# Kernel tuning notes

Hardware: AMD Instinct MI355X
Metric: run time of the kernel (lower is better)

Reference implementation:

```python
import jax, jax.numpy as jnp
import numpy as np


def setup_inputs() -> dict:
    key = jax.random.key(0)
    k1, k2, k3, k4 = jax.random.split(key, 4)
    N, E, D = 50000, 800000, 256
    x = jax.random.normal(k1, (N, D), dtype=jnp.float32)
    edge_index = jax.random.randint(k2, (2, E), 0, N, dtype=jnp.int64)
    W = jax.random.normal(k3, (D, D), dtype=jnp.float32) * (1.0 / np.sqrt(D))
    b_conv = jnp.zeros((D,), dtype=jnp.float32)
    w_lin = jax.random.normal(k4, (1, D), dtype=jnp.float32) * (1.0 / np.sqrt(D))
    b_lin = jnp.zeros((1,), dtype=jnp.float32)
    return {"x": x, "edge_index": edge_index, "W": W, "b_conv": b_conv,
            "w_lin": w_lin, "b_lin": b_lin}


def reference(x, edge_index, W, b_conv, w_lin, b_lin):
    N = x.shape[0]
    # GCNConv with add_self_loops=True, symmetric normalization
    loop = jnp.arange(N, dtype=edge_index.dtype)
    row = jnp.concatenate([edge_index[0], loop])  # source
    col = jnp.concatenate([edge_index[1], loop])  # target
    ones = jnp.ones(row.shape[0], dtype=x.dtype)
    deg = jax.ops.segment_sum(ones, col, num_segments=N)
    deg_inv_sqrt = jnp.where(deg > 0, jax.lax.rsqrt(deg), 0.0)
    norm = deg_inv_sqrt[row] * deg_inv_sqrt[col]  # [E+N]
    h = x @ W                                      # [N, D]
    msg = h[row] * norm[:, None]                   # [E+N, D]
    agg = jax.ops.segment_sum(msg, col, num_segments=N) + b_conv  # [N, D]
    x1 = jax.nn.sigmoid(agg)
    # dropout is identity in eval mode
    x3 = jnp.mean(x1, axis=0)                      # [D]
    x4 = jax.nn.sigmoid(x3 @ w_lin.T + b_lin)      # [1]
    return x4
```

## Files before the change

### kernel.cpp

```cpp
#include <hip/hip_runtime.h>
#include <hip/hip_bf16.h>
#include <stdint.h>

typedef short bf16x8 __attribute__((ext_vector_type(8)));
typedef unsigned short u16x8 __attribute__((ext_vector_type(8)));
typedef float f32x4 __attribute__((ext_vector_type(4)));

static __device__ __forceinline__ unsigned short f32_to_bf16_bits(float f) {
    union { float f; uint32_t u; } v; v.f = f;
    uint32_t lsb = (v.u >> 16) & 1u;
    uint32_t r = v.u + 0x7fffu + lsb;
    return (unsigned short)(r >> 16);
}
static __device__ __forceinline__ float bf16_bits_to_f32(unsigned short u) {
    union { uint32_t u; float f; } v; v.u = ((uint32_t)u) << 16;
    return v.f;
}

__global__ void count_kernel(const int* __restrict__ col, int* __restrict__ cnt, int E) {
    int e = blockIdx.x * blockDim.x + threadIdx.x;
    if (e < E) atomicAdd(&cnt[col[e]], 1);
}

__global__ void scanA_kernel(const int* __restrict__ cnt, int* __restrict__ off,
                             int* __restrict__ bsums, int N) {
    int tid = threadIdx.x;
    int b = blockIdx.x;
    int i0 = b * 1024 + tid * 4;
    int v0 = (i0 + 0 < N) ? cnt[i0 + 0] : 0;
    int v1 = (i0 + 1 < N) ? cnt[i0 + 1] : 0;
    int v2 = (i0 + 2 < N) ? cnt[i0 + 2] : 0;
    int v3 = (i0 + 3 < N) ? cnt[i0 + 3] : 0;
    int s = v0 + v1 + v2 + v3;
    int lane = tid & 63, wid = tid >> 6;
    int inc = s;
    for (int d = 1; d < 64; d <<= 1) {
        int o = __shfl_up(inc, d, 64);
        if (lane >= d) inc += o;
    }
    __shared__ int wt[4];
    if (lane == 63) wt[wid] = inc;
    __syncthreads();
    int wbase = 0;
    for (int k = 0; k < wid; k++) wbase += wt[k];
    int excl = wbase + inc - s;
    if (i0 + 0 < N) off[i0 + 0] = excl;
    if (i0 + 1 < N) off[i0 + 1] = excl + v0;
    if (i0 + 2 < N) off[i0 + 2] = excl + v0 + v1;
    if (i0 + 3 < N) off[i0 + 3] = excl + v0 + v1 + v2;
    if (tid == 255) bsums[b] = wbase + inc;
}

__global__ void scanB_kernel(const int* __restrict__ bsums, int* __restrict__ bbase, int nb) {
    int t = threadIdx.x;
    int s = (t < nb) ? bsums[t] : 0;
    int inc = s;
    for (int d = 1; d < 64; d <<= 1) {
        int o = __shfl_up(inc, d, 64);
        if (t >= d) inc += o;
    }
    if (t < nb) bbase[t] = inc - s;
}

__global__ void scanC_kernel(int* __restrict__ off, int* __restrict__ cursor,
                             float* __restrict__ dis, const int* __restrict__ cnt,
                             const int* __restrict__ bbase, int N, int E) {
    int i = blockIdx.x * blockDim.x + threadIdx.x;
    if (i < N) {
        int o = off[i] + bbase[i >> 10];
        off[i] = o;
        cursor[i] = o;
        dis[i] = rsqrtf((float)(cnt[i] + 1));
    }
    if (i == 0) off[N] = E;
}

__global__ void scatter_kernel(const int* __restrict__ ei, int* __restrict__ cursor,
                               int* __restrict__ srow, int E) {
    int e = blockIdx.x * blockDim.x + threadIdx.x;
    if (e < E) {
        int r = ei[e];
        int c = ei[E + e];
        int p = atomicAdd(&cursor[c], 1);
        srow[p] = r;
    }
}

__global__ __launch_bounds__(256) void xconv_kernel(const float* __restrict__ x,
                                                    unsigned short* __restrict__ xb, int total8) {
    int stride = gridDim.x * blockDim.x;
    for (int i = blockIdx.x * blockDim.x + threadIdx.x; i < total8; i += stride) {
        const float* p = x + (size_t)i * 8;
        float4 a = *(const float4*)p;
        float4 b = *(const float4*)(p + 4);
        u16x8 o;
        o[0] = f32_to_bf16_bits(a.x); o[1] = f32_to_bf16_bits(a.y);
        o[2] = f32_to_bf16_bits(a.z); o[3] = f32_to_bf16_bits(a.w);
        o[4] = f32_to_bf16_bits(b.x); o[5] = f32_to_bf16_bits(b.y);
        o[6] = f32_to_bf16_bits(b.z); o[7] = f32_to_bf16_bits(b.w);
        *(u16x8*)(xb + (size_t)i * 8) = o;
    }
}

__global__ void wprep_kernel(const float* __restrict__ W, unsigned short* __restrict__ Wb) {
    int e = blockIdx.x * blockDim.x + threadIdx.x;
    int k = e >> 8, n = e & 255;
    Wb[(((k >> 3) * 256 + n) << 3) + (k & 7)] = f32_to_bf16_bits(W[e]);
}

__global__ __launch_bounds__(256) void gemm_kernel(const unsigned short* __restrict__ xb,
                                                   const unsigned short* __restrict__ Wb,
                                                   unsigned short* __restrict__ h, int N) {
    int tid = threadIdx.x;
    int lane = tid & 63;
    int w = tid >> 6;
    int l15 = lane & 15, l4 = lane >> 4;
    int m0 = blockIdx.x * 64;
    int colbase = w * 64;

    f32x4 acc[4][4];
    for (int mi = 0; mi < 4; mi++)
        for (int ni = 0; ni < 4; ni++)
            acc[mi][ni] = (f32x4){0.f, 0.f, 0.f, 0.f};

    for (int kk = 0; kk < 8; kk++) {
        bf16x8 a[4], bb[4];
        int k0 = kk * 32 + l4 * 8;
        for (int mi = 0; mi < 4; mi++) {
            int row = m0 + mi * 16 + l15;
            if (row >= N) row = N - 1;
            a[mi] = *(const bf16x8*)(xb + (size_t)row * 256 + k0);
        }
        int kc = kk * 4 + l4;
        for (int ni = 0; ni < 4; ni++) {
            int n = colbase + ni * 16 + l15;
            bb[ni] = *(const bf16x8*)(Wb + (((kc << 8) + n) << 3));
        }
        for (int mi = 0; mi < 4; mi++)
            for (int ni = 0; ni < 4; ni++)
                acc[mi][ni] = __builtin_amdgcn_mfma_f32_16x16x32_bf16(a[mi], bb[ni], acc[mi][ni], 0, 0, 0);
    }

    __shared__ unsigned short tile[4 * 64 * 72];
    unsigned short* tw = tile + w * 64 * 72;
    for (int mi = 0; mi < 4; mi++)
        for (int ni = 0; ni < 4; ni++)
            for (int v = 0; v < 4; v++)
                tw[(mi * 16 + l4 * 4 + v) * 72 + ni * 16 + l15] = f32_to_bf16_bits(acc[mi][ni][v]);
    __builtin_amdgcn_s_waitcnt(0);
    for (int t = 0; t < 8; t++) {
        int row_r = t * 8 + (lane >> 3);
        int col_r = (lane & 7) * 8;
        int gr = m0 + row_r;
        if (gr < N) {
            u16x8 vv = *(const u16x8*)(tw + row_r * 72 + col_r);
            *(u16x8*)(h + (size_t)gr * 256 + colbase + col_r) = vv;
        }
    }
}

__global__ __launch_bounds__(256) void agg_kernel(const unsigned short* __restrict__ h,
                                                  const int* __restrict__ off,
                                                  const int* __restrict__ srow,
                                                  const float* __restrict__ dis,
                                                  const float* __restrict__ bconv,
                                                  float* __restrict__ partials, int N) {
    int lane = threadIdx.x & 63, wid = threadIdx.x >> 6;
    int hi = lane >> 5;
    int l5 = lane & 31;
    int c8 = l5 * 8;
    float bc[8];
    {
        float4 b0 = *(const float4*)(bconv + c8);
        float4 b1 = *(const float4*)(bconv + c8 + 4);
        bc[0]=b0.x; bc[1]=b0.y; bc[2]=b0.z; bc[3]=b0.w;
        bc[4]=b1.x; bc[5]=b1.y; bc[6]=b1.z; bc[7]=b1.w;
    }
    int gw = blockIdx.x * 4 + wid;
    int stride = gridDim.x * 4;

    float m[8];
    for (int k = 0; k < 8; k++) m[k] = 0.f;

    for (int c = gw; c < N; c += stride) {
        float dc = dis[c];
        float a[8];
        {
            float half_dc = 0.5f * dc;
            bf16x8 e = *(const bf16x8*)(h + (size_t)c * 256 + c8);
            for (int k = 0; k < 8; k++) a[k] = half_dc * bf16_bits_to_f32((unsigned short)e[k]);
        }
        int j1 = off[c + 1];
        for (int j = off[c] + hi; j < j1; j += 2) {
            int r = srow[j];
            float wr = dis[r];
            bf16x8 e = *(const bf16x8*)(h + (size_t)r * 256 + c8);
            for (int k = 0; k < 8; k++) a[k] += wr * bf16_bits_to_f32((unsigned short)e[k]);
        }
        for (int k = 0; k < 8; k++) {
            float comb = a[k] + __shfl_xor(a[k], 32);
            float val = comb * dc + bc[k];
            m[k] += 1.f / (1.f + __expf(-val));
        }
    }
    __shared__ float red[4][256];
    if (hi == 0)
        for (int k = 0; k < 8; k++) red[wid][c8 + k] = m[k];
    __syncthreads();
    int d = threadIdx.x;
    partials[(size_t)blockIdx.x * 256 + d] = red[0][d] + red[1][d] + red[2][d] + red[3][d];
}

__global__ void reduceA_kernel(const float* __restrict__ partials, float* __restrict__ p2) {
    int d = threadIdx.x;
    int b = blockIdx.x;
    float s = 0.f;
    int r0 = b * 64;
    for (int r = r0; r < r0 + 64; r++) s += partials[r * 256 + d];
    p2[b * 256 + d] = s;
}

__global__ void final_kernel(const float* __restrict__ p2, const float* __restrict__ wlin,
                             const float* __restrict__ blin, float* __restrict__ out, int N) {
    int d = threadIdx.x;
    float s = 0.f;
    for (int b = 0; b < 32; b++) s += p2[b * 256 + d];
    float x3 = s / (float)N;
    float t = x3 * wlin[d];
    __shared__ float red[256];
    red[d] = t;
    __syncthreads();
    for (int st = 128; st > 0; st >>= 1) {
        if (d < st) red[d] += red[d + st];
        __syncthreads();
    }
    if (d == 0) out[0] = 1.f / (1.f + expf(-(red[0] + blin[0])));
}

extern "C" void kernel_launch(void* const* d_in, const int* in_sizes, int n_in,
                              void* d_out, int out_size, void* d_ws, size_t ws_size,
                              hipStream_t stream) {
    const float* x     = (const float*)d_in[0];
    const int*   ei    = (const int*)d_in[1];
    const float* W     = (const float*)d_in[2];
    const float* bconv = (const float*)d_in[3];
    const float* wlin  = (const float*)d_in[4];
    const float* blin  = (const float*)d_in[5];
    float* out = (float*)d_out;

    int N = in_sizes[0] / 256;
    int E = in_sizes[1] / 2;

    char* ws = (char*)d_ws;
    size_t o = 0;
    auto alloc = [&](size_t bytes) -> char* {
        char* p = ws + o;
        o = (o + bytes + 255) & ~(size_t)255;
        return p;
    };
    int*   cnt     = (int*)alloc((size_t)N * 4);
    int*   off     = (int*)alloc((size_t)(N + 1) * 4);
    int*   cursor  = (int*)alloc((size_t)N * 4);
    float* dis     = (float*)alloc((size_t)N * 4);
    int*   bsums   = (int*)alloc(64 * 4);
    int*   bbase   = (int*)alloc(64 * 4);
    int*   srow    = (int*)alloc((size_t)E * 4);
    unsigned short* Wb = (unsigned short*)alloc(65536 * 2);
    unsigned short* xb = (unsigned short*)alloc((size_t)N * 256 * 2);
    unsigned short* h  = (unsigned short*)alloc((size_t)N * 256 * 2);
    float* partials = (float*)alloc(2048 * 256 * 4);
    float* p2       = (float*)alloc(32 * 256 * 4);

    hipMemsetAsync(cnt, 0, (size_t)N * 4, stream);

    int eb = (E + 255) / 256;
    count_kernel<<<eb, 256, 0, stream>>>(ei + E, cnt, E);

    int nbA = (N + 1023) / 1024;
    scanA_kernel<<<nbA, 256, 0, stream>>>(cnt, off, bsums, N);
    scanB_kernel<<<1, 64, 0, stream>>>(bsums, bbase, nbA);
    scanC_kernel<<<(N + 255) / 256, 256, 0, stream>>>(off, cursor, dis, cnt, bbase, N, E);
    scatter_kernel<<<eb, 256, 0, stream>>>(ei, cursor, srow, E);

    xconv_kernel<<<1024, 256, 0, stream>>>(x, xb, N * 256 / 8);
    wprep_kernel<<<65536 / 256, 256, 0, stream>>>(W, Wb);
    gemm_kernel<<<(N + 63) / 64, 256, 0, stream>>>(xb, Wb, h, N);

    agg_kernel<<<2048, 256, 0, stream>>>(h, off, srow, dis, bconv, partials, N);
    reduceA_kernel<<<32, 256, 0, stream>>>(partials, p2);
    final_kernel<<<1, 256, 0, stream>>>(p2, wlin, blin, out, N);
}
```

Measured before the change: 291.9 us.

## Prescale GEMM output by source norm and widen edge parallelism in aggregation

The GEMM epilogue now multiplies each output row by its deg^-1/2 factor before the bf16 store. This removes the per-edge dis[r] gather and multiply from the aggregation loop. The aggregation kernel is also restructured: each wave splits into four 16-lane groups, each lane covers 16 columns, and each group keeps two edges in flight with separate accumulators, so up to eight neighbor rows load concurrently per wave. The groups are combined with cross-lane shuffles, and each group finishes the sigmoid for a quarter of its columns; in exchange the kernel uses more registers and rounds the norm-scaled values to bf16.

After: 289.9 us. No clear change (-0.7%).

```diff
diff --git a/kernel.cpp b/kernel.cpp
--- a/kernel.cpp
+++ b/kernel.cpp
@@ -110,6 +110,7 @@
 
 __global__ __launch_bounds__(256) void gemm_kernel(const unsigned short* __restrict__ xb,
                                                    const unsigned short* __restrict__ Wb,
+                                                   const float* __restrict__ dis,
                                                    unsigned short* __restrict__ h, int N) {
     int tid = threadIdx.x;
     int lane = tid & 63;
@@ -143,10 +144,17 @@
 
     __shared__ unsigned short tile[4 * 64 * 72];
     unsigned short* tw = tile + w * 64 * 72;
-    for (int mi = 0; mi < 4; mi++)
+    for (int mi = 0; mi < 4; mi++) {
+        float dsc[4];
+        for (int v = 0; v < 4; v++) {
+            int rr = m0 + mi * 16 + l4 * 4 + v;
+            dsc[v] = dis[rr < N ? rr : N - 1];
+        }
         for (int ni = 0; ni < 4; ni++)
             for (int v = 0; v < 4; v++)
-                tw[(mi * 16 + l4 * 4 + v) * 72 + ni * 16 + l15] = f32_to_bf16_bits(acc[mi][ni][v]);
+                tw[(mi * 16 + l4 * 4 + v) * 72 + ni * 16 + l15] =
+                    f32_to_bf16_bits(acc[mi][ni][v] * dsc[v]);
+    }
     __builtin_amdgcn_s_waitcnt(0);
     for (int t = 0; t < 8; t++) {
         int row_r = t * 8 + (lane >> 3);
@@ -166,46 +174,71 @@
                                                   const float* __restrict__ bconv,
                                                   float* __restrict__ partials, int N) {
     int lane = threadIdx.x & 63, wid = threadIdx.x >> 6;
-    int hi = lane >> 5;
-    int l5 = lane & 31;
-    int c8 = l5 * 8;
-    float bc[8];
-    {
-        float4 b0 = *(const float4*)(bconv + c8);
-        float4 b1 = *(const float4*)(bconv + c8 + 4);
-        bc[0]=b0.x; bc[1]=b0.y; bc[2]=b0.z; bc[3]=b0.w;
-        bc[4]=b1.x; bc[5]=b1.y; bc[6]=b1.z; bc[7]=b1.w;
-    }
+    int g = lane >> 4;
+    int q = lane & 15;
+    int c16 = q * 16;
+    float4 bc = *(const float4*)(bconv + c16 + g * 4);
+
     int gw = blockIdx.x * 4 + wid;
     int stride = gridDim.x * 4;
 
-    float m[8];
-    for (int k = 0; k < 8; k++) m[k] = 0.f;
+    float m[4] = {0.f, 0.f, 0.f, 0.f};
 
     for (int c = gw; c < N; c += stride) {
         float dc = dis[c];
-        float a[8];
+        float a[16], b[16];
         {
-            float half_dc = 0.5f * dc;
-            bf16x8 e = *(const bf16x8*)(h + (size_t)c * 256 + c8);
-            for (int k = 0; k < 8; k++) a[k] = half_dc * bf16_bits_to_f32((unsigned short)e[k]);
+            const unsigned short* hp = h + (size_t)c * 256 + c16;
+            bf16x8 e0 = *(const bf16x8*)hp;
+            bf16x8 e1 = *(const bf16x8*)(hp + 8);
+            float sel = (g == 0) ? 1.f : 0.f;
+            for (int k = 0; k < 8; k++) {
+                a[k]     = sel * bf16_bits_to_f32((unsigned short)e0[k]);
+                a[k + 8] = sel * bf16_bits_to_f32((unsigned short)e1[k]);
+                b[k] = 0.f; b[k + 8] = 0.f;
+            }
         }
         int j1 = off[c + 1];
-        for (int j = off[c] + hi; j < j1; j += 2) {
-            int r = srow[j];
-            float wr = dis[r];
-            bf16x8 e = *(const bf16x8*)(h + (size_t)r * 256 + c8);
-            for (int k = 0; k < 8; k++) a[k] += wr * bf16_bits_to_f32((unsigned short)e[k]);
-        }
-        for (int k = 0; k < 8; k++) {
-            float comb = a[k] + __shfl_xor(a[k], 32);
-            float val = comb * dc + bc[k];
-            m[k] += 1.f / (1.f + __expf(-val));
+        int j = off[c] + g;
+        for (; j + 4 < j1; j += 8) {
+            int r0 = srow[j];
+            int r1 = srow[j + 4];
+            const unsigned short* p0 = h + (size_t)r0 * 256 + c16;
+            const unsigned short* p1 = h + (size_t)r1 * 256 + c16;
+            bf16x8 e0 = *(const bf16x8*)p0;
+            bf16x8 e1 = *(const bf16x8*)(p0 + 8);
+            bf16x8 f0 = *(const bf16x8*)p1;
+            bf16x8 f1 = *(const bf16x8*)(p1 + 8);
+            for (int k = 0; k < 8; k++) {
+                a[k]     += bf16_bits_to_f32((unsigned short)e0[k]);
+                a[k + 8] += bf16_bits_to_f32((unsigned short)e1[k]);
+                b[k]     += bf16_bits_to_f32((unsigned short)f0[k]);
+                b[k + 8] += bf16_bits_to_f32((unsigned short)f1[k]);
+            }
+        }
+        if (j < j1) {
+            int r0 = srow[j];
+            const unsigned short* p0 = h + (size_t)r0 * 256 + c16;
+            bf16x8 e0 = *(const bf16x8*)p0;
+            bf16x8 e1 = *(const bf16x8*)(p0 + 8);
+            for (int k = 0; k < 8; k++) {
+                a[k]     += bf16_bits_to_f32((unsigned short)e0[k]);
+                a[k + 8] += bf16_bits_to_f32((unsigned short)e1[k]);
+            }
+        }
+        for (int k = 0; k < 16; k++) {
+            float s = a[k] + b[k];
+            s += __shfl_xor(s, 16);
+            s += __shfl_xor(s, 32);
+            a[k] = s;
+        }
+        for (int t = 0; t < 4; t++) {
+            float val = a[g * 4 + t] * dc + ((const float*)&bc)[t];
+            m[t] += 1.f / (1.f + __expf(-val));
         }
     }
     __shared__ float red[4][256];
-    if (hi == 0)
-        for (int k = 0; k < 8; k++) red[wid][c8 + k] = m[k];
+    for (int t = 0; t < 4; t++) red[wid][c16 + g * 4 + t] = m[t];
     __syncthreads();
     int d = threadIdx.x;
     partials[(size_t)blockIdx.x * 256 + d] = red[0][d] + red[1][d] + red[2][d] + red[3][d];
@@ -284,7 +317,7 @@
 
     xconv_kernel<<<1024, 256, 0, stream>>>(x, xb, N * 256 / 8);
     wprep_kernel<<<65536 / 256, 256, 0, stream>>>(W, Wb);
-    gemm_kernel<<<(N + 63) / 64, 256, 0, stream>>>(xb, Wb, h, N);
+    gemm_kernel<<<(N + 63) / 64, 256, 0, stream>>>(xb, Wb, dis, h, N);
 
     agg_kernel<<<2048, 256, 0, stream>>>(h, off, srow, dis, bconv, partials, N);
     reduceA_kernel<<<32, 256, 0, stream>>>(partials, p2);
```
